# Kernel optimization log

Hardware: AMD Instinct MI355X
Metric: run time of the kernel (lower is better)

## Reference

```python
import jax, jax.numpy as jnp
import numpy as np

S, B_BOX, N_CLASS = 7, 2, 20
L_COORD, L_NOOBJ = 5.0, 0.5
BATCH = 4096
C = 5 * B_BOX + N_CLASS  # 30


def setup_inputs() -> dict:
    key = jax.random.key(0)
    k1, k2, k3, k4 = jax.random.split(key, 4)
    # coords/w/h/classes strictly positive (sqrt is applied to raw values)
    y = jax.random.uniform(k1, (BATCH, S, S, C), minval=0.05, maxval=0.95, dtype=jnp.float32)
    # confidence channels must be exactly 0/1 (mask tests == 1)
    conf0 = jax.random.bernoulli(k3, 0.3, (BATCH, S, S)).astype(jnp.float32)
    conf1 = jax.random.bernoulli(k4, 0.3, (BATCH, S, S)).astype(jnp.float32)
    y = y.at[..., 0].set(conf0).at[..., 5].set(conf1)
    y_h = jax.random.uniform(k2, (BATCH, S, S, C), minval=0.05, maxval=0.95, dtype=jnp.float32)
    return {"y": y, "y_h": y_h}


def _loss(y, y_h):
    b_sz = y.shape[0]
    conf_idx = np.arange(B_BOX) * 5  # [0, 5]
    y_conf = y[..., conf_idx]        # [B,S,S,b]
    yh_conf = y_h[..., conf_idx]
    mf = (y_conf == 1.0).astype(y.dtype)  # obj mask per box, constant wrt grads
    dconf = (y_conf - yh_conf) ** 2
    loss_obj = jnp.sum(dconf * mf)
    loss_noobj = jnp.sum(dconf * (1.0 - mf))

    loss_coord = jnp.zeros((), y.dtype)
    loss_prob = jnp.zeros((), y.dtype)
    for k in range(B_BOX):  # static small loop over boxes
        mk = mf[..., k]  # [B,S,S]
        base = 5 * k
        dxy = (y[..., base + 1] - y_h[..., base + 1]) ** 2 \
            + (y[..., base + 2] - y_h[..., base + 2]) ** 2
        dwh = (jnp.sqrt(y[..., base + 3]) - jnp.sqrt(y_h[..., base + 3])) ** 2 \
            + (jnp.sqrt(y[..., base + 4]) - jnp.sqrt(y_h[..., base + 4])) ** 2
        loss_coord = loss_coord + jnp.sum((dxy + dwh) * mk)

        # prob term: slice from k*5+5 to end (faithful to original, for k=0 this
        # includes box-2's 5 entries), softmax over the masked batch dimension.
        tail = y[..., base + 5:]
        tail_h = y_h[..., base + 5:]
        mkb = mk[..., None]  # [B,S,S,1]
        neg = jnp.where(mkb > 0, tail_h, -jnp.inf)
        m = jnp.max(neg, axis=0)                       # [S,S,Ct]
        m_safe = jnp.where(jnp.isfinite(m), m, 0.0)    # guard empty columns
        p = jnp.exp(tail_h - m_safe) * mkb
        denom = jnp.sum(p, axis=0)
        sm = p / jnp.where(denom > 0, denom, 1.0)
        loss_prob = loss_prob + jnp.sum((tail - sm) ** 2 * mkb)

    loss = loss_obj + L_NOOBJ * loss_noobj + L_COORD * loss_coord + loss_prob
    return loss / b_sz


def reference(y, y_h):
    return _loss(y, y_h)
```

## Files before the change

### kernel.cpp

```cpp
#include <hip/hip_runtime.h>
#include <math.h>

#define CC 30
#define NBATCH 4096
#define NIJ 49
#define NPAIR 1225
#define PSTR 7352
#define THREADS 512
#define SLABF4 1470


__global__ __launch_bounds__(THREADS)
void yolo_main(const float* __restrict__ y, const float* __restrict__ yh,
               float* __restrict__ scal, float* __restrict__ parts, int nwg)
{
    __shared__ float tY[4 * 1470];
    __shared__ float tH[4 * 1470];
    __shared__ float scr[4][8];

    const int tid = threadIdx.x;
    const int wg  = blockIdx.x;
    const int bpw = NBATCH / nwg;
    const int nslab = bpw >> 2;

    const int i0 = tid, i1 = tid + 512;
    const int i2r = tid + 1024;
    const int i2  = (i2r < SLABF4) ? i2r : (SLABF4 - 1);
    const bool w2 = (i2r < SLABF4);

    int  ijv[3], cv[3], pr[3];
    bool val[3];
    #pragma unroll
    for (int i = 0; i < 3; i++) {
        int p = tid + i * THREADS;
        val[i] = (p < NPAIR);
        pr[i]  = p;
        int pp = val[i] ? p : 0;
        ijv[i] = pp / 25;
        cv[i]  = 5 + pp % 25;
    }

    float D0[3] = {0,0,0}, B0[3] = {0,0,0}, C0[3] = {0,0,0};
    float D1[3] = {0,0,0}, B1[3] = {0,0,0}, C1[3] = {0,0,0};
    float obj = 0.f, noobj = 0.f, coord = 0.f, tt = 0.f;

    const float4* Yg = (const float4*)y;
    const float4* Hg = (const float4*)yh;
    float4* tY4 = (float4*)tY;
    float4* tH4 = (float4*)tH;

    {
        const size_t f4 = (size_t)((wg * bpw) >> 2) * SLABF4;
        float4 a0 = Yg[f4+i0], a1 = Yg[f4+i1], a2 = Yg[f4+i2];
        float4 b0 = Hg[f4+i0], b1 = Hg[f4+i1], b2 = Hg[f4+i2];
        tY4[i0] = a0; tY4[i1] = a1; if (w2) tY4[i2] = a2;
        tH4[i0] = b0; tH4[i1] = b1; if (w2) tH4[i2] = b2;
    }
    __syncthreads();

    float4 ry0, ry1, ry2, rh0, rh1, rh2;

    for (int s = 0; s < nslab; s++) {
        if (s + 1 < nslab) {
            const size_t nf4 = (size_t)((wg * bpw + (s+1)*4) >> 2) * SLABF4;
            ry0 = Yg[nf4+i0]; ry1 = Yg[nf4+i1]; ry2 = Yg[nf4+i2];
            rh0 = Hg[nf4+i0]; rh1 = Hg[nf4+i1]; rh2 = Hg[nf4+i2];
        }

        if (tid < 4 * NIJ) {
            const int base = tid * CC;
            float y0 = tY[base],     h0 = tH[base];
            float y5 = tY[base + 5], h5 = tH[base + 5];
            float d0 = y0 - h0; d0 *= d0;
            float d5 = y5 - h5; d5 *= d5;
            const bool m0 = (y0 == 1.0f), m1 = (y5 == 1.0f);
            obj   += (m0 ? d0 : 0.f) + (m1 ? d5 : 0.f);
            noobj += (m0 ? 0.f : d0) + (m1 ? 0.f : d5);
            if (m0) {
                float a  = tY[base + 1] - tH[base + 1];
                float b2 = tY[base + 2] - tH[base + 2];
                float c1 = sqrtf(tY[base + 3]) - sqrtf(tH[base + 3]);
                float c2 = sqrtf(tY[base + 4]) - sqrtf(tH[base + 4]);
                coord += a * a + b2 * b2 + c1 * c1 + c2 * c2;
            }
            if (m1) {
                float a  = tY[base + 6] - tH[base + 6];
                float b2 = tY[base + 7] - tH[base + 7];
                float c1 = sqrtf(tY[base + 8]) - sqrtf(tH[base + 8]);
                float c2 = sqrtf(tY[base + 9]) - sqrtf(tH[base + 9]);
                coord += a * a + b2 * b2 + c1 * c1 + c2 * c2;
            }
        }

        #pragma unroll
        for (int b = 0; b < 4; b++) {
            #pragma unroll
            for (int i = 0; i < 3; i++) {
                if (!val[i]) continue;
                const int cb = b * 1470 + ijv[i] * CC;
                const float w0 = (tY[cb] == 1.0f) ? 1.f : 0.f;
                const float w1 = (cv[i] >= 10 && tY[cb + 5] == 1.0f) ? 1.f : 0.f;
                const float t  = tY[cb + cv[i]];
                const float th = tH[cb + cv[i]];
                const float e  = __expf(th);
                const float te = t * e, ee = e * e, t2 = t * t;
                D0[i] = fmaf(e,  w0, D0[i]);
                B0[i] = fmaf(te, w0, B0[i]);
                C0[i] = fmaf(ee, w0, C0[i]);
                D1[i] = fmaf(e,  w1, D1[i]);
                B1[i] = fmaf(te, w1, B1[i]);
                C1[i] = fmaf(ee, w1, C1[i]);
                tt = fmaf(t2, w0 + w1, tt);
            }
        }
        __syncthreads();
        if (s + 1 < nslab) {
            tY4[i0] = ry0; tY4[i1] = ry1; if (w2) tY4[i2] = ry2;
            tH4[i0] = rh0; tH4[i1] = rh1; if (w2) tH4[i2] = rh2;
        }
        __syncthreads();
    }

    float* pp = parts + (size_t)wg * PSTR;
    #pragma unroll
    for (int i = 0; i < 3; i++) {
        if (!val[i]) continue;
        const int p = pr[i];
        pp[p]            = D0[i];
        pp[NPAIR + p]    = B0[i];
        pp[2*NPAIR + p]  = C0[i];
        pp[3*NPAIR + p]  = D1[i];
        pp[4*NPAIR + p]  = B1[i];
        pp[5*NPAIR + p]  = C1[i];
    }

    const int lane = tid & 63, wv = tid >> 6;
    #pragma unroll
    for (int off = 32; off > 0; off >>= 1) {
        obj   += __shfl_down(obj,   off);
        noobj += __shfl_down(noobj, off);
        coord += __shfl_down(coord, off);
        tt    += __shfl_down(tt,    off);
    }
    if (lane == 0) { scr[0][wv] = obj; scr[1][wv] = noobj; scr[2][wv] = coord; scr[3][wv] = tt; }
    __syncthreads();
    if (tid < 4) {
        float sacc = 0.f;
        #pragma unroll
        for (int w = 0; w < THREADS / 64; w++) sacc += scr[tid][w];
        scal[wg * 4 + tid] = sacc;
    }
}

__global__ __launch_bounds__(512)
void yolo_reduce(const float* __restrict__ parts, float* __restrict__ parts2, int nwg)
{
    const int lane = threadIdx.x & 63;
    const int sub  = threadIdx.x >> 6;
    const int f4i  = blockIdx.x * 64 + lane;
    const int cy   = blockIdx.y;
    const int wpc  = nwg >> 3;
    const int wps  = wpc >> 3;

    float4 s = make_float4(0.f, 0.f, 0.f, 0.f);
    if (f4i < PSTR / 4) {
        const float* q = parts + (size_t)(cy * wpc + sub * wps) * PSTR + f4i * 4;
        for (int w = 0; w < wps; ++w) {
            float4 a = *(const float4*)q;
            s.x += a.x; s.y += a.y; s.z += a.z; s.w += a.w;
            q += PSTR;
        }
    }
    __shared__ float4 sred[8][64];
    sred[sub][lane] = s;
    __syncthreads();
    if (threadIdx.x < 64 && f4i < PSTR / 4) {
        float4 t = sred[0][lane];
        #pragma unroll
        for (int c = 1; c < 8; c++) {
            float4 a = sred[c][lane];
            t.x += a.x; t.y += a.y; t.z += a.z; t.w += a.w;
        }
        *(float4*)(parts2 + (size_t)cy * PSTR + f4i * 4) = t;
    }
}

__global__ __launch_bounds__(1024)
void yolo_final(const float* __restrict__ parts2, const float* __restrict__ scal,
                float* __restrict__ out, int nwg)
{
    float v = 0.f;

    for (int s = threadIdx.x; s < NPAIR; s += 1024) {
        const int cidx = s % 25;
        float D0 = 0, B0 = 0, C0 = 0, D1 = 0, B1 = 0, C1 = 0;
        #pragma unroll
        for (int c = 0; c < 8; c++) {
            const float* t = parts2 + (size_t)c * PSTR;
            D0 += t[s];           B0 += t[NPAIR + s];   C0 += t[2*NPAIR + s];
            D1 += t[3*NPAIR + s]; B1 += t[4*NPAIR + s]; C1 += t[5*NPAIR + s];
        }
        if (D0 > 0.f) v += C0 / (D0 * D0) - 2.f * B0 / D0;
        if (cidx >= 5 && D1 > 0.f) v += C1 / (D1 * D1) - 2.f * B1 / D1;
    }

    const float4* s4 = (const float4*)scal;
    for (int w = threadIdx.x; w < nwg; w += 1024) {
        float4 a = s4[w];
        v += a.x + 0.5f * a.y + 5.0f * a.z + a.w;
    }

    __shared__ float sred[16];
    #pragma unroll
    for (int off = 32; off > 0; off >>= 1) v += __shfl_down(v, off);
    const int lane = threadIdx.x & 63, wv = threadIdx.x >> 6;
    if (lane == 0) sred[wv] = v;
    __syncthreads();
    if (threadIdx.x == 0) {
        float tot = 0.f;
        #pragma unroll
        for (int w = 0; w < 16; w++) tot += sred[w];
        out[0] = tot / (float)NBATCH;
    }
}

extern "C" void kernel_launch(void* const* d_in, const int* in_sizes, int n_in,
                              void* d_out, int out_size, void* d_ws, size_t ws_size,
                              hipStream_t stream)
{
    const float* y  = (const float*)d_in[0];
    const float* yh = (const float*)d_in[1];
    float* out    = (float*)d_out;
    float* scal   = (float*)d_ws;
    float* parts2 = (float*)((char*)d_ws + 4096);
    float* parts  = (float*)((char*)d_ws + 239616);

    const size_t per_wg = (size_t)PSTR * sizeof(float);
    int nwg;
    if      (ws_size >= 239616 + 256 * per_wg) nwg = 256;
    else if (ws_size >= 239616 + 128 * per_wg) nwg = 128;
    else                                       nwg = 64;

    yolo_main<<<nwg, THREADS, 0, stream>>>(y, yh, scal, parts, nwg);
    dim3 g2((PSTR / 4 + 63) / 64, 8);
    yolo_reduce<<<g2, 512, 0, stream>>>(parts, parts2, nwg);
    yolo_final<<<1, 1024, 0, stream>>>(parts2, scal, out, nwg);
}
```

Before: 27.87 us.

## Fuse partial-sum reduction into main kernel via grid-wide flag barrier

```diff
diff --git a/kernel.cpp b/kernel.cpp
--- a/kernel.cpp
+++ b/kernel.cpp
@@ -6,17 +6,21 @@
 #define NIJ 49
 #define NPAIR 1225
 #define PSTR 7352
+#define F4TOT (PSTR / 4)
 #define THREADS 512
 #define SLABF4 1470
+#define TOKEN 0x7E57C0DE
 
 
 __global__ __launch_bounds__(THREADS)
-void yolo_main(const float* __restrict__ y, const float* __restrict__ yh,
-               float* __restrict__ scal, float* __restrict__ parts, int nwg)
+void yolo_fused(const float* __restrict__ y, const float* __restrict__ yh,
+                int* __restrict__ flags, float* __restrict__ sc,
+                float* __restrict__ tbl, float* __restrict__ parts, int nwg)
 {
-    __shared__ float tY[4 * 1470];
-    __shared__ float tH[4 * 1470];
+    __shared__ __align__(16) float tY[4 * 1470];
+    __shared__ __align__(16) float tH[4 * 1470];
     __shared__ float scr[4][8];
+    __shared__ float scrw[4];
 
     const int tid = threadIdx.x;
     const int wg  = blockIdx.x;
@@ -148,67 +152,76 @@
         float sacc = 0.f;
         #pragma unroll
         for (int w = 0; w < THREADS / 64; w++) sacc += scr[tid][w];
-        scal[wg * 4 + tid] = sacc;
+        const float wts[4] = {1.f, 0.5f, 5.f, 1.f};
+        scrw[tid] = sacc * wts[tid];
+    }
+    __syncthreads();
+    if (tid == 0) sc[wg] = scrw[0] + scrw[1] + scrw[2] + scrw[3];
+
+    __syncthreads();
+    __threadfence();
+    if (tid == 0)
+        __hip_atomic_store(&flags[wg], TOKEN, __ATOMIC_RELEASE, __HIP_MEMORY_SCOPE_AGENT);
+    for (int f = tid; f < nwg; f += THREADS) {
+        while (__hip_atomic_load(&flags[f], __ATOMIC_ACQUIRE, __HIP_MEMORY_SCOPE_AGENT) != TOKEN)
+            __builtin_amdgcn_s_sleep(1);
+    }
+    __threadfence();
+    __syncthreads();
+
+    const int F4PB = (F4TOT + nwg - 1) / nwg;
+    float4* sacc4 = (float4*)tY;
+    const float4* parts4 = (const float4*)parts;
+    float4* tbl4 = (float4*)tbl;
+
+    for (int pass = 0; pass < (F4PB + 7) / 8; pass++) {
+        const int k = pass * 8 + (tid & 7);
+        const int f = wg * F4PB + k;
+        float4 sv = make_float4(0.f, 0.f, 0.f, 0.f);
+        if (k < F4PB && f < F4TOT) {
+            const float4* q = parts4 + (size_t)(tid >> 3) * F4TOT + f;
+            for (int r = tid >> 3; r < nwg; r += 64) {
+                float4 a = *q;
+                sv.x += a.x; sv.y += a.y; sv.z += a.z; sv.w += a.w;
+                q += (size_t)64 * F4TOT;
+            }
+        }
+        sacc4[tid] = sv;
+        __syncthreads();
+        #pragma unroll
+        for (int off = 256; off >= 8; off >>= 1) {
+            if (tid < off) {
+                float4 a = sacc4[tid], b = sacc4[tid + off];
+                a.x += b.x; a.y += b.y; a.z += b.z; a.w += b.w;
+                sacc4[tid] = a;
+            }
+            __syncthreads();
+        }
+        if (tid < 8) {
+            const int kk = pass * 8 + tid;
+            const int ff = wg * F4PB + kk;
+            if (kk < F4PB && ff < F4TOT) tbl4[ff] = sacc4[tid];
+        }
+        __syncthreads();
     }
 }
 
-__global__ __launch_bounds__(512)
-void yolo_reduce(const float* __restrict__ parts, float* __restrict__ parts2, int nwg)
-{
-    const int lane = threadIdx.x & 63;
-    const int sub  = threadIdx.x >> 6;
-    const int f4i  = blockIdx.x * 64 + lane;
-    const int cy   = blockIdx.y;
-    const int wpc  = nwg >> 3;
-    const int wps  = wpc >> 3;
-
-    float4 s = make_float4(0.f, 0.f, 0.f, 0.f);
-    if (f4i < PSTR / 4) {
-        const float* q = parts + (size_t)(cy * wpc + sub * wps) * PSTR + f4i * 4;
-        for (int w = 0; w < wps; ++w) {
-            float4 a = *(const float4*)q;
-            s.x += a.x; s.y += a.y; s.z += a.z; s.w += a.w;
-            q += PSTR;
-        }
-    }
-    __shared__ float4 sred[8][64];
-    sred[sub][lane] = s;
-    __syncthreads();
-    if (threadIdx.x < 64 && f4i < PSTR / 4) {
-        float4 t = sred[0][lane];
-        #pragma unroll
-        for (int c = 1; c < 8; c++) {
-            float4 a = sred[c][lane];
-            t.x += a.x; t.y += a.y; t.z += a.z; t.w += a.w;
-        }
-        *(float4*)(parts2 + (size_t)cy * PSTR + f4i * 4) = t;
-    }
-}
-
 __global__ __launch_bounds__(1024)
-void yolo_final(const float* __restrict__ parts2, const float* __restrict__ scal,
-                float* __restrict__ out, int nwg)
+void yolo_final(const float* __restrict__ tbl, const float* __restrict__ sc,
+                int* __restrict__ flags, float* __restrict__ out, int nwg)
 {
     float v = 0.f;
 
     for (int s = threadIdx.x; s < NPAIR; s += 1024) {
         const int cidx = s % 25;
-        float D0 = 0, B0 = 0, C0 = 0, D1 = 0, B1 = 0, C1 = 0;
-        #pragma unroll
-        for (int c = 0; c < 8; c++) {
-            const float* t = parts2 + (size_t)c * PSTR;
-            D0 += t[s];           B0 += t[NPAIR + s];   C0 += t[2*NPAIR + s];
-            D1 += t[3*NPAIR + s]; B1 += t[4*NPAIR + s]; C1 += t[5*NPAIR + s];
-        }
+        float D0 = tbl[s], B0 = tbl[NPAIR + s], C0 = tbl[2*NPAIR + s];
         if (D0 > 0.f) v += C0 / (D0 * D0) - 2.f * B0 / D0;
-        if (cidx >= 5 && D1 > 0.f) v += C1 / (D1 * D1) - 2.f * B1 / D1;
-    }
-
-    const float4* s4 = (const float4*)scal;
-    for (int w = threadIdx.x; w < nwg; w += 1024) {
-        float4 a = s4[w];
-        v += a.x + 0.5f * a.y + 5.0f * a.z + a.w;
-    }
+        if (cidx >= 5) {
+            float D1 = tbl[3*NPAIR + s], B1 = tbl[4*NPAIR + s], C1 = tbl[5*NPAIR + s];
+            if (D1 > 0.f) v += C1 / (D1 * D1) - 2.f * B1 / D1;
+        }
+    }
+    for (int w = threadIdx.x; w < nwg; w += 1024) v += sc[w];
 
     __shared__ float sred[16];
     #pragma unroll
@@ -222,6 +235,7 @@
         for (int w = 0; w < 16; w++) tot += sred[w];
         out[0] = tot / (float)NBATCH;
     }
+    if (threadIdx.x < 256) flags[threadIdx.x] = 0;
 }
 
 extern "C" void kernel_launch(void* const* d_in, const int* in_sizes, int n_in,
@@ -230,19 +244,18 @@
 {
     const float* y  = (const float*)d_in[0];
     const float* yh = (const float*)d_in[1];
-    float* out    = (float*)d_out;
-    float* scal   = (float*)d_ws;
-    float* parts2 = (float*)((char*)d_ws + 4096);
-    float* parts  = (float*)((char*)d_ws + 239616);
+    float* out   = (float*)d_out;
+    int*   flags = (int*)d_ws;
+    float* sc    = (float*)((char*)d_ws + 4096);
+    float* tbl   = (float*)((char*)d_ws + 8192);
+    float* parts = (float*)((char*)d_ws + 49152);
 
     const size_t per_wg = (size_t)PSTR * sizeof(float);
     int nwg;
-    if      (ws_size >= 239616 + 256 * per_wg) nwg = 256;
-    else if (ws_size >= 239616 + 128 * per_wg) nwg = 128;
-    else                                       nwg = 64;
-
-    yolo_main<<<nwg, THREADS, 0, stream>>>(y, yh, scal, parts, nwg);
-    dim3 g2((PSTR / 4 + 63) / 64, 8);
-    yolo_reduce<<<g2, 512, 0, stream>>>(parts, parts2, nwg);
-    yolo_final<<<1, 1024, 0, stream>>>(parts2, scal, out, nwg);
+    if      (ws_size >= 49152 + 256 * per_wg) nwg = 256;
+    else if (ws_size >= 49152 + 128 * per_wg) nwg = 128;
+    else                                      nwg = 64;
+
+    yolo_fused<<<nwg, THREADS, 0, stream>>>(y, yh, flags, sc, tbl, parts, nwg);
+    yolo_final<<<1, 1024, 0, stream>>>(tbl, sc, flags, out, nwg);
 }
```

Result: slower. 105.8 us (+279.4%).

## Read y_h directly from global memory and double the workgroup count

Applied to the files above, without the earlier changes.

```diff
diff --git a/kernel.cpp b/kernel.cpp
--- a/kernel.cpp
+++ b/kernel.cpp
@@ -6,6 +6,7 @@
 #define NIJ 49
 #define NPAIR 1225
 #define PSTR 7352
+#define F4TOT (PSTR / 4)
 #define THREADS 512
 #define SLABF4 1470
 
@@ -14,8 +15,7 @@
 void yolo_main(const float* __restrict__ y, const float* __restrict__ yh,
                float* __restrict__ scal, float* __restrict__ parts, int nwg)
 {
-    __shared__ float tY[4 * 1470];
-    __shared__ float tH[4 * 1470];
+    __shared__ __align__(16) float tY[4 * 1470];
     __shared__ float scr[4][8];
 
     const int tid = threadIdx.x;
@@ -45,49 +45,47 @@
     float obj = 0.f, noobj = 0.f, coord = 0.f, tt = 0.f;
 
     const float4* Yg = (const float4*)y;
-    const float4* Hg = (const float4*)yh;
     float4* tY4 = (float4*)tY;
-    float4* tH4 = (float4*)tH;
 
     {
         const size_t f4 = (size_t)((wg * bpw) >> 2) * SLABF4;
         float4 a0 = Yg[f4+i0], a1 = Yg[f4+i1], a2 = Yg[f4+i2];
-        float4 b0 = Hg[f4+i0], b1 = Hg[f4+i1], b2 = Hg[f4+i2];
         tY4[i0] = a0; tY4[i1] = a1; if (w2) tY4[i2] = a2;
-        tH4[i0] = b0; tH4[i1] = b1; if (w2) tH4[i2] = b2;
-    }
-    __syncthreads();
-
-    float4 ry0, ry1, ry2, rh0, rh1, rh2;
+    }
+    __syncthreads();
+
+    float4 ry0, ry1, ry2;
 
     for (int s = 0; s < nslab; s++) {
+        const size_t gslab = (size_t)(wg * bpw + s * 4) * 1470;
+
         if (s + 1 < nslab) {
             const size_t nf4 = (size_t)((wg * bpw + (s+1)*4) >> 2) * SLABF4;
             ry0 = Yg[nf4+i0]; ry1 = Yg[nf4+i1]; ry2 = Yg[nf4+i2];
-            rh0 = Hg[nf4+i0]; rh1 = Hg[nf4+i1]; rh2 = Hg[nf4+i2];
         }
 
         if (tid < 4 * NIJ) {
             const int base = tid * CC;
-            float y0 = tY[base],     h0 = tH[base];
-            float y5 = tY[base + 5], h5 = tH[base + 5];
+            const float* hq = yh + gslab + base;
+            float y0 = tY[base],     h0 = hq[0];
+            float y5 = tY[base + 5], h5 = hq[5];
             float d0 = y0 - h0; d0 *= d0;
             float d5 = y5 - h5; d5 *= d5;
             const bool m0 = (y0 == 1.0f), m1 = (y5 == 1.0f);
             obj   += (m0 ? d0 : 0.f) + (m1 ? d5 : 0.f);
             noobj += (m0 ? 0.f : d0) + (m1 ? 0.f : d5);
             if (m0) {
-                float a  = tY[base + 1] - tH[base + 1];
-                float b2 = tY[base + 2] - tH[base + 2];
-                float c1 = sqrtf(tY[base + 3]) - sqrtf(tH[base + 3]);
-                float c2 = sqrtf(tY[base + 4]) - sqrtf(tH[base + 4]);
+                float a  = tY[base + 1] - hq[1];
+                float b2 = tY[base + 2] - hq[2];
+                float c1 = sqrtf(tY[base + 3]) - sqrtf(hq[3]);
+                float c2 = sqrtf(tY[base + 4]) - sqrtf(hq[4]);
                 coord += a * a + b2 * b2 + c1 * c1 + c2 * c2;
             }
             if (m1) {
-                float a  = tY[base + 6] - tH[base + 6];
-                float b2 = tY[base + 7] - tH[base + 7];
-                float c1 = sqrtf(tY[base + 8]) - sqrtf(tH[base + 8]);
-                float c2 = sqrtf(tY[base + 9]) - sqrtf(tH[base + 9]);
+                float a  = tY[base + 6] - hq[6];
+                float b2 = tY[base + 7] - hq[7];
+                float c1 = sqrtf(tY[base + 8]) - sqrtf(hq[8]);
+                float c2 = sqrtf(tY[base + 9]) - sqrtf(hq[9]);
                 coord += a * a + b2 * b2 + c1 * c1 + c2 * c2;
             }
         }
@@ -101,7 +99,7 @@
                 const float w0 = (tY[cb] == 1.0f) ? 1.f : 0.f;
                 const float w1 = (cv[i] >= 10 && tY[cb + 5] == 1.0f) ? 1.f : 0.f;
                 const float t  = tY[cb + cv[i]];
-                const float th = tH[cb + cv[i]];
+                const float th = yh[gslab + cb + cv[i]];
                 const float e  = __expf(th);
                 const float te = t * e, ee = e * e, t2 = t * t;
                 D0[i] = fmaf(e,  w0, D0[i]);
@@ -116,7 +114,6 @@
         __syncthreads();
         if (s + 1 < nslab) {
             tY4[i0] = ry0; tY4[i1] = ry1; if (w2) tY4[i2] = ry2;
-            tH4[i0] = rh0; tH4[i1] = rh1; if (w2) tH4[i2] = rh2;
         }
         __syncthreads();
     }
@@ -163,7 +160,7 @@
     const int wps  = wpc >> 3;
 
     float4 s = make_float4(0.f, 0.f, 0.f, 0.f);
-    if (f4i < PSTR / 4) {
+    if (f4i < F4TOT) {
         const float* q = parts + (size_t)(cy * wpc + sub * wps) * PSTR + f4i * 4;
         for (int w = 0; w < wps; ++w) {
             float4 a = *(const float4*)q;
@@ -174,7 +171,7 @@
     __shared__ float4 sred[8][64];
     sred[sub][lane] = s;
     __syncthreads();
-    if (threadIdx.x < 64 && f4i < PSTR / 4) {
+    if (threadIdx.x < 64 && f4i < F4TOT) {
         float4 t = sred[0][lane];
         #pragma unroll
         for (int c = 1; c < 8; c++) {
@@ -232,17 +229,17 @@
     const float* yh = (const float*)d_in[1];
     float* out    = (float*)d_out;
     float* scal   = (float*)d_ws;
-    float* parts2 = (float*)((char*)d_ws + 4096);
-    float* parts  = (float*)((char*)d_ws + 239616);
+    float* parts2 = (float*)((char*)d_ws + 8192);
+    float* parts  = (float*)((char*)d_ws + 243456);
 
     const size_t per_wg = (size_t)PSTR * sizeof(float);
     int nwg;
-    if      (ws_size >= 239616 + 256 * per_wg) nwg = 256;
-    else if (ws_size >= 239616 + 128 * per_wg) nwg = 128;
-    else                                       nwg = 64;
+    if      (ws_size >= 243456 + 512 * per_wg) nwg = 512;
+    else if (ws_size >= 243456 + 256 * per_wg) nwg = 256;
+    else                                       nwg = 128;
 
     yolo_main<<<nwg, THREADS, 0, stream>>>(y, yh, scal, parts, nwg);
-    dim3 g2((PSTR / 4 + 63) / 64, 8);
+    dim3 g2((F4TOT + 63) / 64, 8);
     yolo_reduce<<<g2, 512, 0, stream>>>(parts, parts2, nwg);
     yolo_final<<<1, 1024, 0, stream>>>(parts2, scal, out, nwg);
 }
```

Result: slower. 31.51 us (+13.0%).

## Double main-kernel block size and collapse two-level partial reduction into one

Applied to the files above, without the earlier changes.

```diff
diff --git a/kernel.cpp b/kernel.cpp
--- a/kernel.cpp
+++ b/kernel.cpp
@@ -6,7 +6,8 @@
 #define NIJ 49
 #define NPAIR 1225
 #define PSTR 7352
-#define THREADS 512
+#define F4TOT (PSTR / 4)
+#define THREADS 1024
 #define SLABF4 1470
 
 
@@ -14,24 +15,24 @@
 void yolo_main(const float* __restrict__ y, const float* __restrict__ yh,
                float* __restrict__ scal, float* __restrict__ parts, int nwg)
 {
-    __shared__ float tY[4 * 1470];
-    __shared__ float tH[4 * 1470];
-    __shared__ float scr[4][8];
+    __shared__ __align__(16) float tY[4 * 1470];
+    __shared__ __align__(16) float tH[4 * 1470];
+    __shared__ float scr[4][16];
 
     const int tid = threadIdx.x;
     const int wg  = blockIdx.x;
     const int bpw = NBATCH / nwg;
     const int nslab = bpw >> 2;
 
-    const int i0 = tid, i1 = tid + 512;
-    const int i2r = tid + 1024;
-    const int i2  = (i2r < SLABF4) ? i2r : (SLABF4 - 1);
-    const bool w2 = (i2r < SLABF4);
-
-    int  ijv[3], cv[3], pr[3];
-    bool val[3];
-    #pragma unroll
-    for (int i = 0; i < 3; i++) {
+    const int i0 = tid;
+    const int i1r = tid + 1024;
+    const int i1  = (i1r < SLABF4) ? i1r : (SLABF4 - 1);
+    const bool w1 = (i1r < SLABF4);
+
+    int  ijv[2], cv[2], pr[2];
+    bool val[2];
+    #pragma unroll
+    for (int i = 0; i < 2; i++) {
         int p = tid + i * THREADS;
         val[i] = (p < NPAIR);
         pr[i]  = p;
@@ -40,8 +41,8 @@
         cv[i]  = 5 + pp % 25;
     }
 
-    float D0[3] = {0,0,0}, B0[3] = {0,0,0}, C0[3] = {0,0,0};
-    float D1[3] = {0,0,0}, B1[3] = {0,0,0}, C1[3] = {0,0,0};
+    float D0[2] = {0,0}, B0[2] = {0,0}, C0[2] = {0,0};
+    float D1[2] = {0,0}, B1[2] = {0,0}, C1[2] = {0,0};
     float obj = 0.f, noobj = 0.f, coord = 0.f, tt = 0.f;
 
     const float4* Yg = (const float4*)y;
@@ -51,20 +52,20 @@
 
     {
         const size_t f4 = (size_t)((wg * bpw) >> 2) * SLABF4;
-        float4 a0 = Yg[f4+i0], a1 = Yg[f4+i1], a2 = Yg[f4+i2];
-        float4 b0 = Hg[f4+i0], b1 = Hg[f4+i1], b2 = Hg[f4+i2];
-        tY4[i0] = a0; tY4[i1] = a1; if (w2) tY4[i2] = a2;
-        tH4[i0] = b0; tH4[i1] = b1; if (w2) tH4[i2] = b2;
-    }
-    __syncthreads();
-
-    float4 ry0, ry1, ry2, rh0, rh1, rh2;
+        float4 a0 = Yg[f4+i0], a1 = Yg[f4+i1];
+        float4 b0 = Hg[f4+i0], b1 = Hg[f4+i1];
+        tY4[i0] = a0; if (w1) tY4[i1] = a1;
+        tH4[i0] = b0; if (w1) tH4[i1] = b1;
+    }
+    __syncthreads();
+
+    float4 ry0, ry1, rh0, rh1;
 
     for (int s = 0; s < nslab; s++) {
         if (s + 1 < nslab) {
             const size_t nf4 = (size_t)((wg * bpw + (s+1)*4) >> 2) * SLABF4;
-            ry0 = Yg[nf4+i0]; ry1 = Yg[nf4+i1]; ry2 = Yg[nf4+i2];
-            rh0 = Hg[nf4+i0]; rh1 = Hg[nf4+i1]; rh2 = Hg[nf4+i2];
+            ry0 = Yg[nf4+i0]; ry1 = Yg[nf4+i1];
+            rh0 = Hg[nf4+i0]; rh1 = Hg[nf4+i1];
         }
 
         if (tid < 4 * NIJ) {
@@ -95,11 +96,11 @@
         #pragma unroll
         for (int b = 0; b < 4; b++) {
             #pragma unroll
-            for (int i = 0; i < 3; i++) {
+            for (int i = 0; i < 2; i++) {
                 if (!val[i]) continue;
                 const int cb = b * 1470 + ijv[i] * CC;
                 const float w0 = (tY[cb] == 1.0f) ? 1.f : 0.f;
-                const float w1 = (cv[i] >= 10 && tY[cb + 5] == 1.0f) ? 1.f : 0.f;
+                const float wk = (cv[i] >= 10 && tY[cb + 5] == 1.0f) ? 1.f : 0.f;
                 const float t  = tY[cb + cv[i]];
                 const float th = tH[cb + cv[i]];
                 const float e  = __expf(th);
@@ -107,23 +108,23 @@
                 D0[i] = fmaf(e,  w0, D0[i]);
                 B0[i] = fmaf(te, w0, B0[i]);
                 C0[i] = fmaf(ee, w0, C0[i]);
-                D1[i] = fmaf(e,  w1, D1[i]);
-                B1[i] = fmaf(te, w1, B1[i]);
-                C1[i] = fmaf(ee, w1, C1[i]);
-                tt = fmaf(t2, w0 + w1, tt);
+                D1[i] = fmaf(e,  wk, D1[i]);
+                B1[i] = fmaf(te, wk, B1[i]);
+                C1[i] = fmaf(ee, wk, C1[i]);
+                tt = fmaf(t2, w0 + wk, tt);
             }
         }
         __syncthreads();
         if (s + 1 < nslab) {
-            tY4[i0] = ry0; tY4[i1] = ry1; if (w2) tY4[i2] = ry2;
-            tH4[i0] = rh0; tH4[i1] = rh1; if (w2) tH4[i2] = rh2;
+            tY4[i0] = ry0; if (w1) tY4[i1] = ry1;
+            tH4[i0] = rh0; if (w1) tH4[i1] = rh1;
         }
         __syncthreads();
     }
 
     float* pp = parts + (size_t)wg * PSTR;
     #pragma unroll
-    for (int i = 0; i < 3; i++) {
+    for (int i = 0; i < 2; i++) {
         if (!val[i]) continue;
         const int p = pr[i];
         pp[p]            = D0[i];
@@ -153,18 +154,16 @@
 }
 
 __global__ __launch_bounds__(512)
-void yolo_reduce(const float* __restrict__ parts, float* __restrict__ parts2, int nwg)
+void yolo_reduce(const float* __restrict__ parts, float* __restrict__ tbl, int nwg)
 {
     const int lane = threadIdx.x & 63;
     const int sub  = threadIdx.x >> 6;
     const int f4i  = blockIdx.x * 64 + lane;
-    const int cy   = blockIdx.y;
-    const int wpc  = nwg >> 3;
-    const int wps  = wpc >> 3;
+    const int wps  = nwg >> 3;
 
     float4 s = make_float4(0.f, 0.f, 0.f, 0.f);
-    if (f4i < PSTR / 4) {
-        const float* q = parts + (size_t)(cy * wpc + sub * wps) * PSTR + f4i * 4;
+    if (f4i < F4TOT) {
+        const float* q = parts + (size_t)(sub * wps) * PSTR + f4i * 4;
         for (int w = 0; w < wps; ++w) {
             float4 a = *(const float4*)q;
             s.x += a.x; s.y += a.y; s.z += a.z; s.w += a.w;
@@ -174,36 +173,32 @@
     __shared__ float4 sred[8][64];
     sred[sub][lane] = s;
     __syncthreads();
-    if (threadIdx.x < 64 && f4i < PSTR / 4) {
+    if (threadIdx.x < 64 && f4i < F4TOT) {
         float4 t = sred[0][lane];
         #pragma unroll
         for (int c = 1; c < 8; c++) {
             float4 a = sred[c][lane];
             t.x += a.x; t.y += a.y; t.z += a.z; t.w += a.w;
         }
-        *(float4*)(parts2 + (size_t)cy * PSTR + f4i * 4) = t;
+        *(float4*)(tbl + f4i * 4) = t;
     }
 }
 
 __global__ __launch_bounds__(1024)
-void yolo_final(const float* __restrict__ parts2, const float* __restrict__ scal,
+void yolo_final(const float* __restrict__ tbl, const float* __restrict__ scal,
                 float* __restrict__ out, int nwg)
 {
     float v = 0.f;
 
     for (int s = threadIdx.x; s < NPAIR; s += 1024) {
         const int cidx = s % 25;
-        float D0 = 0, B0 = 0, C0 = 0, D1 = 0, B1 = 0, C1 = 0;
-        #pragma unroll
-        for (int c = 0; c < 8; c++) {
-            const float* t = parts2 + (size_t)c * PSTR;
-            D0 += t[s];           B0 += t[NPAIR + s];   C0 += t[2*NPAIR + s];
-            D1 += t[3*NPAIR + s]; B1 += t[4*NPAIR + s]; C1 += t[5*NPAIR + s];
-        }
+        float D0 = tbl[s], B0 = tbl[NPAIR + s], C0 = tbl[2*NPAIR + s];
         if (D0 > 0.f) v += C0 / (D0 * D0) - 2.f * B0 / D0;
-        if (cidx >= 5 && D1 > 0.f) v += C1 / (D1 * D1) - 2.f * B1 / D1;
-    }
-
+        if (cidx >= 5) {
+            float D1 = tbl[3*NPAIR + s], B1 = tbl[4*NPAIR + s], C1 = tbl[5*NPAIR + s];
+            if (D1 > 0.f) v += C1 / (D1 * D1) - 2.f * B1 / D1;
+        }
+    }
     const float4* s4 = (const float4*)scal;
     for (int w = threadIdx.x; w < nwg; w += 1024) {
         float4 a = s4[w];
@@ -230,19 +225,18 @@
 {
     const float* y  = (const float*)d_in[0];
     const float* yh = (const float*)d_in[1];
-    float* out    = (float*)d_out;
-    float* scal   = (float*)d_ws;
-    float* parts2 = (float*)((char*)d_ws + 4096);
-    float* parts  = (float*)((char*)d_ws + 239616);
+    float* out   = (float*)d_out;
+    float* scal  = (float*)d_ws;
+    float* tbl   = (float*)((char*)d_ws + 8192);
+    float* parts = (float*)((char*)d_ws + 40960);
 
     const size_t per_wg = (size_t)PSTR * sizeof(float);
     int nwg;
-    if      (ws_size >= 239616 + 256 * per_wg) nwg = 256;
-    else if (ws_size >= 239616 + 128 * per_wg) nwg = 128;
-    else                                       nwg = 64;
+    if      (ws_size >= 40960 + 256 * per_wg) nwg = 256;
+    else if (ws_size >= 40960 + 128 * per_wg) nwg = 128;
+    else                                      nwg = 64;
 
     yolo_main<<<nwg, THREADS, 0, stream>>>(y, yh, scal, parts, nwg);
-    dim3 g2((PSTR / 4 + 63) / 64, 8);
-    yolo_reduce<<<g2, 512, 0, stream>>>(parts, parts2, nwg);
-    yolo_final<<<1, 1024, 0, stream>>>(parts2, scal, out, nwg);
-}
+    yolo_reduce<<<(F4TOT + 63) / 64, 512, 0, stream>>>(parts, tbl, nwg);
+    yolo_final<<<1, 1024, 0, stream>>>(tbl, scal, out, nwg);
+}
```

Measured after the change: 32.97 us. 18.3% more time.
